# Kernel optimization log

Measured on AMD Instinct MI355X. Metric: run time of the kernel, lower is better.

The kernel has to match this reference:

```python
import jax, jax.numpy as jnp
import numpy as np

LP, LQ, B, IN, HID = 256, 256, 32, 512, 512
H = 2 * HID          # internal hidden size (hidden_size * 2)
IN2 = 2 * IN         # Up/Uq feature dim after self-concat
IN4 = 4 * IN


def setup_inputs() -> dict:
    key = jax.random.key(0)
    ks = jax.random.split(key, 12)
    def w(k, shape, fan):
        return (jax.random.normal(k, shape, jnp.float32) / np.float32(np.sqrt(fan)))
    return {
        "up": jax.random.normal(ks[0], (LP, B, IN), jnp.float32),
        "uq": jax.random.normal(ks[1], (LQ, B, IN), jnp.float32),
        "v0": jax.random.normal(ks[2], (B, H), jnp.float32),    # torch.randn v
        "Vvec": jax.random.normal(ks[3], (B, H), jnp.float32),  # torch.randn V (squeezed)
        "Wp": w(ks[4], (H, IN2), IN2),
        "Wq": w(ks[5], (H, IN2), IN2),
        "Wv": w(ks[6], (H, H), H),
        "Wg": w(ks[7], (IN4, IN4), IN4),
        "W_ih": w(ks[8], (3 * H, IN2), IN2),
        "W_hh": w(ks[9], (3 * H, H), H),
        "b_ih": w(ks[10], (3 * H,), H),
        "b_hh": w(ks[11], (3 * H,), H),
    }


def reference(up, uq, v0, Vvec, Wp, Wq, Wv, Wg, W_ih, W_hh, b_ih, b_hh):
    in2 = 2 * up.shape[2]
    # mixer indices are arange -> Up/Uq are just feature self-concats
    Up = jnp.concatenate([up, up], axis=2)   # [lp, B, in2]
    Uq = jnp.concatenate([uq, uq], axis=2)   # [lq, B, in2]
    # hoist loop-invariant projections (original recomputes Wq(Uq) each step)
    WUp = jnp.einsum('pbi,hi->pbh', Up, Wp)  # [lp, B, H]
    WUq = jnp.einsum('qbi,hi->qbh', Uq, Wq)  # [lq, B, H]

    def gru_cell(x, h):
        gi = x @ W_ih.T + b_ih
        gh = h @ W_hh.T + b_hh
        i_r, i_z, i_n = jnp.split(gi, 3, axis=1)
        h_r, h_z, h_n = jnp.split(gh, 3, axis=1)
        r = jax.nn.sigmoid(i_r + h_r)
        z = jax.nn.sigmoid(i_z + h_z)
        n = jnp.tanh(i_n + r * h_n)
        return (1.0 - z) * n + z * h

    def step(v, xs):
        up_i, wup_i = xs                                   # [B,in2], [B,H]
        x = jnp.tanh(wup_i[None] + WUq + (v @ Wv.T)[None])  # [lq, B, H]
        s = jnp.einsum('qbh,bh->bq', x, Vvec)               # [B, lq]
        a = jax.nn.softmax(s, axis=1)
        c = jnp.einsum('bq,qbd->bd', a, Uq)                 # [B, in2]
        r = jnp.concatenate([up_i, c], axis=1)              # [B, in4]
        g = jax.nn.sigmoid(r @ Wg.T)
        c_ = (g * r)[:, in2:]                               # gated context half
        v_new = gru_cell(c_, v)
        return v_new, v_new

    _, vs = jax.lax.scan(step, v0, (Up, WUp))   # vs: [lp, B, H]
    # dropout in eval mode = identity
    return vs
```

## Files before the change

### kernel.cpp

```cpp
#include <hip/hip_runtime.h>


#define NB 32

__device__ __forceinline__ float fsig(float x) { return 1.0f / (1.0f + __expf(-x)); }
__device__ __forceinline__ float ftanh(float x) { return 1.0f - 2.0f / (1.0f + __expf(2.0f * x)); }

__device__ __forceinline__ float wred(float a) {
#pragma unroll
  for (int o = 32; o >= 1; o >>= 1) a += __shfl_xor(a, o, 64);
  return a;
}

__device__ __forceinline__ float cload(const float* p) {
  return __hip_atomic_load(p, __ATOMIC_RELAXED, __HIP_MEMORY_SCOPE_AGENT);
}
__device__ __forceinline__ void cstore(float* p, float v) {
  __hip_atomic_store(p, v, __ATOMIC_RELAXED, __HIP_MEMORY_SCOPE_AGENT);
}

__device__ __forceinline__ void gbar(int* cnt, int target) {
  __syncthreads();
  if (threadIdx.x == 0) {
    __hip_atomic_fetch_add(cnt, 1, __ATOMIC_RELAXED, __HIP_MEMORY_SCOPE_AGENT);
    int spins = 0;
    for (;;) {
      if (__hip_atomic_load(cnt, __ATOMIC_RELAXED, __HIP_MEMORY_SCOPE_AGENT) >= target) break;
      __builtin_amdgcn_s_sleep(8);
      if ((++spins & 255) == 0) {
        if (__hip_atomic_load(cnt, __ATOMIC_ACQUIRE, __HIP_MEMORY_SCOPE_AGENT) >= target) break;
      }
    }
  }
  __syncthreads();
}

__global__ __launch_bounds__(256) void k_init(
    const float* __restrict__ v0, const float* __restrict__ Wp,
    const float* __restrict__ Wg, float* __restrict__ wsbase,
    float* __restrict__ vbuf, float* __restrict__ Wpf, float* __restrict__ Wg2f) {
  int i = blockIdx.x * 256 + threadIdx.x;
  if (i < 64) ((int*)wsbase)[i] = 0;
  if (i < NB * 1024) vbuf[i] = v0[i];
  if (i < 1024 * 512) {
    int n = i >> 9, k = i & 511;
    Wpf[i] = Wp[(size_t)n * 1024 + k] + Wp[(size_t)n * 1024 + k + 512];
  }
  if (i < 1024 * 1024) {
    int j = i >> 10, kk = i & 1023;
    const float* wr = Wg + (size_t)(1024 + j) * 2048;
    Wg2f[i] = (kk < 512) ? (wr[kk] + wr[kk + 512]) : (wr[kk + 512] + wr[kk + 1024]);
  }
}

__global__ __launch_bounds__(256) void k_wuq(
    const float* __restrict__ A, const float* __restrict__ Wq, float* __restrict__ C) {
  __shared__ float As[16][65];
  __shared__ float Bs[16][65];
  int bm = blockIdx.x * 64, bn = blockIdx.y * 64;
  int t = threadIdx.x;
  int tx = t & 15, ty = t >> 4;
  float acc[4][4] = {};
  for (int k0 = 0; k0 < 512; k0 += 16) {
#pragma unroll
    for (int l = 0; l < 4; ++l) {
      int idx = t + l * 256;
      int row = idx >> 4, kk = idx & 15;
      As[kk][row] = A[(size_t)(bm + row) * 512 + k0 + kk];
      Bs[kk][row] = Wq[(size_t)(bn + row) * 1024 + k0 + kk] +
                    Wq[(size_t)(bn + row) * 1024 + k0 + kk + 512];
    }
    __syncthreads();
#pragma unroll
    for (int kk = 0; kk < 16; ++kk) {
      float a0[4], b0[4];
#pragma unroll
      for (int i = 0; i < 4; ++i) a0[i] = As[kk][ty * 4 + i];
#pragma unroll
      for (int j = 0; j < 4; ++j) b0[j] = Bs[kk][tx * 4 + j];
#pragma unroll
      for (int i = 0; i < 4; ++i)
#pragma unroll
        for (int j = 0; j < 4; ++j) acc[i][j] += a0[i] * b0[j];
    }
    __syncthreads();
  }
#pragma unroll
  for (int i = 0; i < 4; ++i)
#pragma unroll
    for (int j = 0; j < 4; ++j)
      C[(size_t)(bm + ty * 4 + i) * 1024 + bn + tx * 4 + j] = acc[i][j];
}

__global__ __launch_bounds__(512, 2) void k_loop(
    const float* __restrict__ up, const float* __restrict__ uq,
    const float* __restrict__ Vvec, const float* __restrict__ Wv,
    const float* __restrict__ W_hh, const float* __restrict__ b_hh,
    const float* __restrict__ W_ih, const float* __restrict__ b_ih,
    float* __restrict__ out, float* __restrict__ ws) {
  int* cnt = (int*)ws;
  float* vbuf  = ws + 64;
  float* tbuf  = ws + 32832;
  float* ghbuf = ws + 65600;
  float* sbuf  = ws + 163904;
  float* chalf = ws + 172096;
  float* cbuf  = ws + 188480;
  float* Wpf   = ws + 221248;
  float* Wg2f  = ws + 745536;
  float* WUq   = ws + 1794112;

  int bid = blockIdx.x;
  int tid = threadIdx.x, lane = tid & 63, wave = tid >> 6;

  __shared__ float smem[12288];

  int s = bid & 63, bg = bid >> 6, b0 = bg * 8;
  bool is_t = (s < 16);
  int b3 = bid >> 3, i0 = (bid & 7) * 64;
  int b2 = bid & 31, qg2 = bid >> 5;

  int ho5 = tid >> 3, bb5 = tid & 7;
  int h5 = s * 16 + ho5, b5 = b0 + bb5;
  float vloc = 0.0f;
  if (tid < 128) vloc = cload(vbuf + (size_t)b5 * 1024 + h5);

  int bar = 0;

  for (int p = 0; p < 256; ++p) {
    {
      for (int idx = tid; idx < 8192; idx += 512)
        smem[idx] = cload(vbuf + (size_t)b0 * 1024 + idx);
      if (is_t) {
        for (int idx = tid; idx < 4096; idx += 512)
          smem[8192 + idx] = up[((size_t)p * NB + b0) * 512 + idx];
      }
      __syncthreads();
      float vreg[8][16];
#pragma unroll
      for (int bb = 0; bb < 8; ++bb)
#pragma unroll
        for (int i = 0; i < 16; ++i)
          vreg[bb][i] = smem[bb * 1024 + lane + i * 64];
      int n0 = s * 64 + wave * 8;
      for (int rr = 0; rr < 8; ++rr) {
        int n = n0 + rr;
        float acc[8];
#pragma unroll
        for (int bb = 0; bb < 8; ++bb) acc[bb] = 0.0f;
        if (is_t) {
          const float* wr = Wv + (size_t)n * 1024;
#pragma unroll
          for (int i = 0; i < 16; ++i) {
            float w = wr[lane + i * 64];
#pragma unroll
            for (int bb = 0; bb < 8; ++bb) acc[bb] = fmaf(w, vreg[bb][i], acc[bb]);
          }
          const float* wp = Wpf + (size_t)n * 512;
#pragma unroll
          for (int i = 0; i < 8; ++i) {
            float w = wp[lane + i * 64];
#pragma unroll
            for (int bb = 0; bb < 8; ++bb)
              acc[bb] = fmaf(w, smem[8192 + bb * 512 + lane + i * 64], acc[bb]);
          }
#pragma unroll
          for (int bb = 0; bb < 8; ++bb) {
            float a = wred(acc[bb]);
            if (lane == 0) cstore(tbuf + (size_t)(b0 + bb) * 1024 + n, a);
          }
        } else {
          int m = n - 1024;
          const float* wr = W_hh + (size_t)m * 1024;
#pragma unroll
          for (int i = 0; i < 16; ++i) {
            float w = wr[lane + i * 64];
#pragma unroll
            for (int bb = 0; bb < 8; ++bb) acc[bb] = fmaf(w, vreg[bb][i], acc[bb]);
          }
          float bias = b_hh[m];
#pragma unroll
          for (int bb = 0; bb < 8; ++bb) {
            float a = wred(acc[bb]);
            if (lane == 0) cstore(ghbuf + (size_t)(b0 + bb) * 3072 + m, a + bias);
          }
        }
      }
    }
    ++bar; gbar(cnt, 256 * bar);

    {
      for (int i = tid; i < 1024; i += 512)
        smem[i] = cload(tbuf + (size_t)b2 * 1024 + i);
      __syncthreads();
      float vvreg[16], treg[16];
#pragma unroll
      for (int i = 0; i < 16; ++i) {
        vvreg[i] = Vvec[(size_t)b2 * 1024 + lane + i * 64];
        treg[i] = smem[lane + i * 64];
      }
      for (int qq = 0; qq < 4; ++qq) {
        int q = qg2 * 32 + wave * 4 + qq;
        const float* wu = WUq + ((size_t)q * NB + b2) * 1024;
        float a = 0.0f;
#pragma unroll
        for (int i = 0; i < 16; ++i)
          a += ftanh(treg[i] + wu[lane + i * 64]) * vvreg[i];
        a = wred(a);
        if (lane == 0) cstore(sbuf + b2 * 256 + q, a);
      }
    }
    ++bar; gbar(cnt, 256 * bar);

    {
      float* a_s  = smem;
      float* red  = smem + 256;
      float* part = smem + 512;
      int b = b3;
      float sv = -1e30f;
      if (tid < 256) sv = cload(sbuf + b * 256 + tid);
      float m = sv;
#pragma unroll
      for (int o = 32; o >= 1; o >>= 1) m = fmaxf(m, __shfl_xor(m, o, 64));
      if (lane == 0 && wave < 4) red[wave] = m;
      __syncthreads();
      float bm = fmaxf(fmaxf(red[0], red[1]), fmaxf(red[2], red[3]));
      __syncthreads();
      float e = 0.0f;
      if (tid < 256) e = __expf(sv - bm);
      float se = e;
#pragma unroll
      for (int o = 32; o >= 1; o >>= 1) se += __shfl_xor(se, o, 64);
      if (lane == 0 && wave < 4) red[wave] = se;
      __syncthreads();
      float tot = red[0] + red[1] + red[2] + red[3];
      if (tid < 256) a_s[tid] = e / tot;
      __syncthreads();
      float acc = 0.0f;
      for (int qq = 0; qq < 32; ++qq) {
        int q = wave * 32 + qq;
        acc += a_s[q] * uq[((size_t)q * NB + b) * 512 + i0 + lane];
      }
      part[wave * 64 + lane] = acc;
      __syncthreads();
      if (tid < 64) {
        float c = 0.0f;
#pragma unroll
        for (int w = 0; w < 8; ++w) c += part[w * 64 + tid];
        cstore(chalf + (size_t)b * 512 + i0 + tid, c);
      }
    }
    ++bar; gbar(cnt, 256 * bar);

    {
      for (int idx = tid; idx < 4096; idx += 512)
        smem[idx] = cload(chalf + (size_t)b0 * 512 + idx);
      __syncthreads();
      float rreg[8][16];
#pragma unroll
      for (int bb = 0; bb < 8; ++bb) {
#pragma unroll
        for (int i = 0; i < 8; ++i)
          rreg[bb][i] = up[((size_t)p * NB + b0 + bb) * 512 + lane + i * 64];
#pragma unroll
        for (int i = 0; i < 8; ++i)
          rreg[bb][8 + i] = smem[bb * 512 + lane + i * 64];
      }
      int j0 = s * 16 + wave * 2;
      for (int rr = 0; rr < 2; ++rr) {
        int j = j0 + rr;
        const float* wr = Wg2f + (size_t)j * 1024;
        float acc[8];
#pragma unroll
        for (int bb = 0; bb < 8; ++bb) acc[bb] = 0.0f;
#pragma unroll
        for (int i = 0; i < 16; ++i) {
          float w = wr[lane + i * 64];
#pragma unroll
          for (int bb = 0; bb < 8; ++bb) acc[bb] = fmaf(w, rreg[bb][i], acc[bb]);
        }
#pragma unroll
        for (int bb = 0; bb < 8; ++bb) {
          float a = wred(acc[bb]);
          if (lane == 0) {
            float cv = smem[bb * 512 + (j & 511)];
            cstore(cbuf + (size_t)(b0 + bb) * 1024 + j, fsig(a) * cv);
          }
        }
      }
    }
    ++bar; gbar(cnt, 256 * bar);

    {
      float ghr = 0.0f, ghz = 0.0f, ghn = 0.0f;
      if (tid < 128) {
        const float* ghb = ghbuf + (size_t)b5 * 3072;
        ghr = cload(ghb + h5);
        ghz = cload(ghb + 1024 + h5);
        ghn = cload(ghb + 2048 + h5);
      }
      for (int idx = tid; idx < 8192; idx += 512)
        smem[idx] = cload(cbuf + (size_t)b0 * 1024 + idx);
      __syncthreads();
      float creg[8][16];
#pragma unroll
      for (int bb = 0; bb < 8; ++bb)
#pragma unroll
        for (int i = 0; i < 16; ++i)
          creg[bb][i] = smem[bb * 1024 + lane + i * 64];
      float* gi_s = smem + 8192;
      for (int k = 0; k < 6; ++k) {
        int idx = wave * 6 + k;
        int g = idx >> 4, ho = idx & 15;
        int r = g * 1024 + s * 16 + ho;
        const float* wr = W_ih + (size_t)r * 1024;
        float acc[8];
#pragma unroll
        for (int bb = 0; bb < 8; ++bb) acc[bb] = 0.0f;
#pragma unroll
        for (int i = 0; i < 16; ++i) {
          float w = wr[lane + i * 64];
#pragma unroll
          for (int bb = 0; bb < 8; ++bb) acc[bb] = fmaf(w, creg[bb][i], acc[bb]);
        }
        float bias = b_ih[r];
#pragma unroll
        for (int bb = 0; bb < 8; ++bb) {
          float a = wred(acc[bb]);
          if (lane == 0) gi_s[idx * 8 + bb] = a + bias;
        }
      }
      __syncthreads();
      if (tid < 128) {
        float gir = gi_s[(0 * 16 + ho5) * 8 + bb5];
        float giz = gi_s[(1 * 16 + ho5) * 8 + bb5];
        float gin = gi_s[(2 * 16 + ho5) * 8 + bb5];
        float rg = fsig(gir + ghr);
        float z  = fsig(giz + ghz);
        float nn = ftanh(gin + rg * ghn);
        float vn = (1.0f - z) * nn + z * vloc;
        vloc = vn;
        cstore(vbuf + (size_t)b5 * 1024 + h5, vn);
        __builtin_nontemporal_store(vn, out + ((size_t)p * NB + b5) * 1024 + h5);
      }
    }
    ++bar; gbar(cnt, 256 * bar);
  }
}

extern "C" void kernel_launch(void* const* d_in, const int* in_sizes, int n_in,
                              void* d_out, int out_size, void* d_ws, size_t ws_size,
                              hipStream_t stream) {
  const float* up = (const float*)d_in[0];
  const float* uq = (const float*)d_in[1];
  const float* v0 = (const float*)d_in[2];
  const float* Vvec = (const float*)d_in[3];
  const float* Wp = (const float*)d_in[4];
  const float* Wq = (const float*)d_in[5];
  const float* Wv = (const float*)d_in[6];
  const float* Wg = (const float*)d_in[7];
  const float* W_ih = (const float*)d_in[8];
  const float* W_hh = (const float*)d_in[9];
  const float* b_ih = (const float*)d_in[10];
  const float* b_hh = (const float*)d_in[11];
  float* out = (float*)d_out;
  float* ws = (float*)d_ws;

  float* vbuf = ws + 64;
  float* Wpf  = ws + 221248;
  float* Wg2f = ws + 745536;
  float* WUq  = ws + 1794112;

  k_init<<<4096, 256, 0, stream>>>(v0, Wp, Wg, ws, vbuf, Wpf, Wg2f);
  k_wuq<<<dim3(128, 16), 256, 0, stream>>>(uq, Wq, WUq);
  k_loop<<<256, 512, 0, stream>>>(up, uq, Vvec, Wv, W_hh, b_hh, W_ih, b_ih, out, ws);
}
```

Before: 30.35 ms.

## Replace grid-wide barrier with per-batch-group hierarchical barriers and remap work locally

Replaces the single global counter barrier over all 256 blocks with barriers scoped to each 64-block batch group. Each group has four sub-counters and a root counter, each padded onto its own cache line. The score and softmax phases are remapped so each block only consumes data produced by blocks in its own batch group, which is what allows the barrier to be scoped this narrowly. Global loads are batched into registers before the shared-memory stores, and the read-only WUq/uq streams use nontemporal loads. The intent is lower contention and latency per barrier across the 256 timesteps, at the cost of a more complex counter layout and dependence on the new data partitioning being correct.

Measured after the change: 32.34 ms. +6.5%, slower.

```diff
diff --git a/kernel.cpp b/kernel.cpp
--- a/kernel.cpp
+++ b/kernel.cpp
@@ -2,6 +2,7 @@
 
 
 #define NB 32
+#define WOFF 16384
 
 __device__ __forceinline__ float fsig(float x) { return 1.0f / (1.0f + __expf(-x)); }
 __device__ __forceinline__ float ftanh(float x) { return 1.0f - 2.0f / (1.0f + __expf(2.0f * x)); }
@@ -18,18 +19,23 @@
 __device__ __forceinline__ void cstore(float* p, float v) {
   __hip_atomic_store(p, v, __ATOMIC_RELAXED, __HIP_MEMORY_SCOPE_AGENT);
 }
-
-__device__ __forceinline__ void gbar(int* cnt, int target) {
+__device__ __forceinline__ int cloadi(const int* p) {
+  return __hip_atomic_load(p, __ATOMIC_RELAXED, __HIP_MEMORY_SCOPE_AGENT);
+}
+
+__device__ __forceinline__ void bgbar(int* sub, int* root, int bar) {
   __syncthreads();
   if (threadIdx.x == 0) {
-    __hip_atomic_fetch_add(cnt, 1, __ATOMIC_RELAXED, __HIP_MEMORY_SCOPE_AGENT);
-    int spins = 0;
+    int old = __hip_atomic_fetch_add(sub, 1, __ATOMIC_RELAXED, __HIP_MEMORY_SCOPE_AGENT);
+    if (old == 16 * bar - 1)
+      __hip_atomic_fetch_add(root, 1, __ATOMIC_RELAXED, __HIP_MEMORY_SCOPE_AGENT);
+    int tgt = 4 * bar, spins = 0;
     for (;;) {
-      if (__hip_atomic_load(cnt, __ATOMIC_RELAXED, __HIP_MEMORY_SCOPE_AGENT) >= target) break;
-      __builtin_amdgcn_s_sleep(8);
-      if ((++spins & 255) == 0) {
-        if (__hip_atomic_load(cnt, __ATOMIC_ACQUIRE, __HIP_MEMORY_SCOPE_AGENT) >= target) break;
-      }
+      if (cloadi(root) >= tgt) break;
+      __builtin_amdgcn_s_sleep(2);
+      if (((++spins) & 255) == 0 &&
+          __hip_atomic_load(root, __ATOMIC_ACQUIRE, __HIP_MEMORY_SCOPE_AGENT) >= tgt)
+        break;
     }
   }
   __syncthreads();
@@ -40,7 +46,7 @@
     const float* __restrict__ Wg, float* __restrict__ wsbase,
     float* __restrict__ vbuf, float* __restrict__ Wpf, float* __restrict__ Wg2f) {
   int i = blockIdx.x * 256 + threadIdx.x;
-  if (i < 64) ((int*)wsbase)[i] = 0;
+  if (i < WOFF) ((int*)wsbase)[i] = 0;
   if (i < NB * 1024) vbuf[i] = v0[i];
   if (i < 1024 * 512) {
     int n = i >> 9, k = i & 511;
@@ -98,16 +104,17 @@
     const float* __restrict__ W_hh, const float* __restrict__ b_hh,
     const float* __restrict__ W_ih, const float* __restrict__ b_ih,
     float* __restrict__ out, float* __restrict__ ws) {
-  int* cnt = (int*)ws;
-  float* vbuf  = ws + 64;
-  float* tbuf  = ws + 32832;
-  float* ghbuf = ws + 65600;
-  float* sbuf  = ws + 163904;
-  float* chalf = ws + 172096;
-  float* cbuf  = ws + 188480;
-  float* Wpf   = ws + 221248;
-  float* Wg2f  = ws + 745536;
-  float* WUq   = ws + 1794112;
+  int* cbase = (int*)ws;
+
+  float* vbuf  = ws + WOFF;
+  float* tbuf  = ws + WOFF + 32768;
+  float* ghbuf = ws + WOFF + 65536;
+  float* sbuf  = ws + WOFF + 163840;
+  float* chalf = ws + WOFF + 172032;
+  float* cbuf  = ws + WOFF + 188416;
+  float* Wpf   = ws + WOFF + 221184;
+  float* Wg2f  = ws + WOFF + 745472;
+  float* WUq   = ws + WOFF + 1794048;
 
   int bid = blockIdx.x;
   int tid = threadIdx.x, lane = tid & 63, wave = tid >> 6;
@@ -116,8 +123,15 @@
 
   int s = bid & 63, bg = bid >> 6, b0 = bg * 8;
   bool is_t = (s < 16);
-  int b3 = bid >> 3, i0 = (bid & 7) * 64;
-  int b2 = bid & 31, qg2 = bid >> 5;
+  int b3 = b0 + (s >> 3), i0 = (s & 7) * 64;
+
+  int* subc = cbase + (bg * 8 + (s >> 4)) * 64;
+  int* rootc = cbase + (bg * 8 + 4) * 64;
+
+  float vvreg[16];
+#pragma unroll
+  for (int i = 0; i < 16; ++i)
+    vvreg[i] = Vvec[(size_t)(b0 + wave) * 1024 + lane + i * 64];
 
   int ho5 = tid >> 3, bb5 = tid & 7;
   int h5 = s * 16 + ho5, b5 = b0 + bb5;
@@ -128,11 +142,19 @@
 
   for (int p = 0; p < 256; ++p) {
     {
-      for (int idx = tid; idx < 8192; idx += 512)
-        smem[idx] = cload(vbuf + (size_t)b0 * 1024 + idx);
+      float tmp[16];
+#pragma unroll
+      for (int i = 0; i < 16; ++i)
+        tmp[i] = cload(vbuf + (size_t)b0 * 1024 + tid + i * 512);
+#pragma unroll
+      for (int i = 0; i < 16; ++i) smem[tid + i * 512] = tmp[i];
       if (is_t) {
-        for (int idx = tid; idx < 4096; idx += 512)
-          smem[8192 + idx] = up[((size_t)p * NB + b0) * 512 + idx];
+        float tu[8];
+#pragma unroll
+        for (int i = 0; i < 8; ++i)
+          tu[i] = up[((size_t)p * NB + b0) * 512 + tid + i * 512];
+#pragma unroll
+        for (int i = 0; i < 8; ++i) smem[8192 + tid + i * 512] = tu[i];
       }
       __syncthreads();
       float vreg[8][16];
@@ -186,30 +208,32 @@
         }
       }
     }
-    ++bar; gbar(cnt, 256 * bar);
+    ++bar; bgbar(subc, rootc, bar);
 
     {
-      for (int i = tid; i < 1024; i += 512)
-        smem[i] = cload(tbuf + (size_t)b2 * 1024 + i);
-      __syncthreads();
-      float vvreg[16], treg[16];
-#pragma unroll
-      for (int i = 0; i < 16; ++i) {
-        vvreg[i] = Vvec[(size_t)b2 * 1024 + lane + i * 64];
-        treg[i] = smem[lane + i * 64];
-      }
+      float tmp[16];
+#pragma unroll
+      for (int i = 0; i < 16; ++i)
+        tmp[i] = cload(tbuf + (size_t)b0 * 1024 + tid + i * 512);
+#pragma unroll
+      for (int i = 0; i < 16; ++i) smem[tid + i * 512] = tmp[i];
+      __syncthreads();
+      float treg[16];
+#pragma unroll
+      for (int i = 0; i < 16; ++i) treg[i] = smem[wave * 1024 + lane + i * 64];
+      int bq = b0 + wave;
       for (int qq = 0; qq < 4; ++qq) {
-        int q = qg2 * 32 + wave * 4 + qq;
-        const float* wu = WUq + ((size_t)q * NB + b2) * 1024;
+        int q = s * 4 + qq;
+        const float* wu = WUq + ((size_t)q * NB + bq) * 1024;
         float a = 0.0f;
 #pragma unroll
         for (int i = 0; i < 16; ++i)
-          a += ftanh(treg[i] + wu[lane + i * 64]) * vvreg[i];
+          a += ftanh(treg[i] + __builtin_nontemporal_load(wu + lane + i * 64)) * vvreg[i];
         a = wred(a);
-        if (lane == 0) cstore(sbuf + b2 * 256 + q, a);
-      }
-    }
-    ++bar; gbar(cnt, 256 * bar);
+        if (lane == 0) cstore(sbuf + bq * 256 + q, a);
+      }
+    }
+    ++bar; bgbar(subc, rootc, bar);
 
     {
       float* a_s  = smem;
@@ -238,7 +262,8 @@
       float acc = 0.0f;
       for (int qq = 0; qq < 32; ++qq) {
         int q = wave * 32 + qq;
-        acc += a_s[q] * uq[((size_t)q * NB + b) * 512 + i0 + lane];
+        acc += a_s[q] *
+               __builtin_nontemporal_load(uq + ((size_t)q * NB + b) * 512 + i0 + lane);
       }
       part[wave * 64 + lane] = acc;
       __syncthreads();
@@ -249,11 +274,15 @@
         cstore(chalf + (size_t)b * 512 + i0 + tid, c);
       }
     }
-    ++bar; gbar(cnt, 256 * bar);
+    ++bar; bgbar(subc, rootc, bar);
 
     {
-      for (int idx = tid; idx < 4096; idx += 512)
-        smem[idx] = cload(chalf + (size_t)b0 * 512 + idx);
+      float tc[8];
+#pragma unroll
+      for (int i = 0; i < 8; ++i)
+        tc[i] = cload(chalf + (size_t)b0 * 512 + tid + i * 512);
+#pragma unroll
+      for (int i = 0; i < 8; ++i) smem[tid + i * 512] = tc[i];
       __syncthreads();
       float rreg[8][16];
 #pragma unroll
@@ -288,7 +317,7 @@
         }
       }
     }
-    ++bar; gbar(cnt, 256 * bar);
+    ++bar; bgbar(subc, rootc, bar);
 
     {
       float ghr = 0.0f, ghz = 0.0f, ghn = 0.0f;
@@ -298,8 +327,12 @@
         ghz = cload(ghb + 1024 + h5);
         ghn = cload(ghb + 2048 + h5);
       }
-      for (int idx = tid; idx < 8192; idx += 512)
-        smem[idx] = cload(cbuf + (size_t)b0 * 1024 + idx);
+      float tmp[16];
+#pragma unroll
+      for (int i = 0; i < 16; ++i)
+        tmp[i] = cload(cbuf + (size_t)b0 * 1024 + tid + i * 512);
+#pragma unroll
+      for (int i = 0; i < 16; ++i) smem[tid + i * 512] = tmp[i];
       __syncthreads();
       float creg[8][16];
 #pragma unroll
@@ -343,7 +376,7 @@
         __builtin_nontemporal_store(vn, out + ((size_t)p * NB + b5) * 1024 + h5);
       }
     }
-    ++bar; gbar(cnt, 256 * bar);
+    ++bar; bgbar(subc, rootc, bar);
   }
 }
 
@@ -365,10 +398,10 @@
   float* out = (float*)d_out;
   float* ws = (float*)d_ws;
 
-  float* vbuf = ws + 64;
-  float* Wpf  = ws + 221248;
-  float* Wg2f = ws + 745536;
-  float* WUq  = ws + 1794112;
+  float* vbuf = ws + WOFF;
+  float* Wpf  = ws + WOFF + 221184;
+  float* Wg2f = ws + WOFF + 745472;
+  float* WUq  = ws + WOFF + 1794048;
 
   k_init<<<4096, 256, 0, stream>>>(v0, Wp, Wg, ws, vbuf, Wpf, Wg2f);
   k_wuq<<<dim3(128, 16), 256, 0, stream>>>(uq, Wq, WUq);
```
